# Kernel tuning notes

Measured on AMD Instinct MI355X. Metric: run time of the kernel, lower is better.

The kernel has to match this reference:

```python
import jax, jax.numpy as jnp
import numpy as np

ALPHA = 1.702
LIMIT = 7.0
TOP_K = 2
B, S, H, E, I = 2, 1024, 768, 8, 768


def setup_inputs() -> dict:
    key = jax.random.key(0)
    ks = jax.random.split(key, 7)
    scale = 0.02
    return {
        "hidden_states": jax.random.normal(ks[0], (B, S, H), dtype=jnp.float32),
        "Wr": jax.random.normal(ks[1], (H, E), dtype=jnp.float32) * scale,
        "br": jax.random.normal(ks[2], (E,), dtype=jnp.float32) * scale,
        "Wgu": jax.random.normal(ks[3], (E, H, 2 * I), dtype=jnp.float32) * scale,
        "bgu": jax.random.normal(ks[4], (E, 2 * I), dtype=jnp.float32) * scale,
        "Wd": jax.random.normal(ks[5], (E, I, H), dtype=jnp.float32) * scale,
        "bd": jax.random.normal(ks[6], (E, H), dtype=jnp.float32) * scale,
    }


def reference(hidden_states, Wr, br, Wgu, bgu, Wd, bd):
    # Router: top-K experts per token, softmax over the K selected logits
    logits = jnp.einsum("bsh,he->bse", hidden_states, Wr) + br
    topk_vals, topk_idx = jax.lax.top_k(logits, TOP_K)        # [B,S,K]
    router_scores = jax.nn.softmax(topk_vals, axis=-1)         # [B,S,K]

    # Dense-over-experts grouped GEMM (sparse_matmul reference: unselected
    # experts are computed but never read by the combine gather below).
    gu = jnp.einsum("bsh,ehf->bsef", hidden_states, Wgu) + bgu  # [B,S,E,2I]
    gu = jnp.minimum(gu, LIMIT)
    gate = gu[..., :I]
    up = jnp.maximum(gu[..., I:], -LIMIT)
    glu = gate * jax.nn.sigmoid(gate * ALPHA)
    activated = (up + 1.0) * glu                                # [B,S,E,I]

    down = jnp.einsum("bsei,eih->bseh", activated, Wd) + bd     # [B,S,E,H]

    # all_to_all_combine (num_devices=1): gather this token's K expert outputs
    sel = jnp.take_along_axis(down, topk_idx[..., None], axis=2)  # [B,S,K,H]
    output = jnp.sum(sel * router_scores[..., None], axis=2)      # [B,S,H]
    return output
```

## Files before the change

kernel.cpp:

```cpp
#include <hip/hip_runtime.h>
#include <hip/hip_bf16.h>
#include <cmath>

#define ALPHA 1.702f
#define LIMIT 7.0f

constexpr int B = 2, S = 1024, H = 768, E = 8, I = 768;
constexpr int T = B * S;
constexpr int TWO_I = 2 * I;
constexpr int CAP = T;
constexpr int NT1 = I / 64;
constexpr int NT2 = H / 64;
constexpr int MT = CAP / 128;

constexpr int RTR_BLKS = 64;
constexpr int WGU_TILES = E * (TWO_I / 64) * (H / 64);
constexpr int WD_TILES  = E * (H / 64) * (H / 64);
constexpr int PRE_BLKS = RTR_BLKS + WGU_TILES + WD_TILES;

typedef __attribute__((ext_vector_type(8))) short short8;
typedef __attribute__((ext_vector_type(4))) float floatx4;

__device__ __forceinline__ unsigned short f2bf(float v) {
  __hip_bfloat16 h = __float2bfloat16(v);
  return *reinterpret_cast<unsigned short*>(&h);
}

__device__ __forceinline__ void g2l16(const void* g, void* l) {
  __builtin_amdgcn_global_load_lds(
      (const __attribute__((address_space(1))) void*)g,
      (__attribute__((address_space(3))) void*)l, 16, 0, 0);
}

__global__ __launch_bounds__(256) void fused_pre(
    const float* __restrict__ x, const float* __restrict__ Wr,
    const float* __restrict__ br, const float* __restrict__ Wgu,
    const float* __restrict__ Wd, unsigned short* __restrict__ Wgt,
    unsigned short* __restrict__ Wdt, unsigned short* __restrict__ xb,
    float* __restrict__ out, int* __restrict__ e_cnt,
    int* __restrict__ row_token, float* __restrict__ row_w) {
  int bid = blockIdx.x;
  int tid = threadIdx.x;

  if (bid < RTR_BLKS) {
    __shared__ int cnt_s[E];
    __shared__ int base_s[E];
    __shared__ int tok_e[E][64];
    __shared__ float wv_e[E][64];

    if (tid < E) cnt_s[tid] = 0;
    __syncthreads();

    int wave = tid >> 6;
    int lane = tid & 63;

    for (int tt = 0; tt < 8; tt++) {
      int t = bid * 32 + wave * 8 + tt;
      const float* xr = x + (size_t)t * H;

      float4 z4 = {0.f, 0.f, 0.f, 0.f};
#pragma unroll
      for (int j = 0; j < 3; j++)
        *(float4*)(out + (size_t)t * H + (size_t)(j * 64 + lane) * 4) = z4;

      float acc[E];
#pragma unroll
      for (int e = 0; e < E; e++) acc[e] = 0.0f;

#pragma unroll
      for (int it = 0; it < 3; it++) {
        int h4 = it * 64 + lane;
        float4 xv = *(const float4*)(xr + (size_t)h4 * 4);
        ushort4 xo;
        xo.x = f2bf(xv.x);
        xo.y = f2bf(xv.y);
        xo.z = f2bf(xv.z);
        xo.w = f2bf(xv.w);
        *(ushort4*)(xb + (size_t)t * H + (size_t)h4 * 4) = xo;
        const float* wrow = Wr + (size_t)h4 * 4 * E;
        float xs[4] = {xv.x, xv.y, xv.z, xv.w};
#pragma unroll
        for (int j = 0; j < 4; j++)
#pragma unroll
          for (int e = 0; e < E; e++) acc[e] += xs[j] * wrow[j * E + e];
      }
#pragma unroll
      for (int e = 0; e < E; e++) {
        float v = acc[e];
        for (int off = 32; off > 0; off >>= 1) v += __shfl_down(v, off, 64);
        acc[e] = v;
      }
      if (lane == 0) {
        float logits[E];
#pragma unroll
        for (int e = 0; e < E; e++) logits[e] = acc[e] + br[e];
        int i0 = 0;
        float v0 = logits[0];
#pragma unroll
        for (int e = 1; e < E; e++)
          if (logits[e] > v0) { v0 = logits[e]; i0 = e; }
        int i1 = -1;
        float v1 = -INFINITY;
#pragma unroll
        for (int e = 0; e < E; e++) {
          if (e == i0) continue;
          if (logits[e] > v1) { v1 = logits[e]; i1 = e; }
        }
        float s1 = __expf(v1 - v0);
        float denom = 1.0f + s1;
        int p0 = atomicAdd(&cnt_s[i0], 1);
        tok_e[i0][p0] = t;
        wv_e[i0][p0] = 1.0f / denom;
        int p1 = atomicAdd(&cnt_s[i1], 1);
        tok_e[i1][p1] = t;
        wv_e[i1][p1] = s1 / denom;
      }
    }
    __syncthreads();
    if (tid < E) base_s[tid] = atomicAdd(&e_cnt[tid], cnt_s[tid]);
    __syncthreads();
#pragma unroll
    for (int e = 0; e < E; e++) {
      int c = cnt_s[e], b0 = base_s[e];
      for (int j = tid; j < c; j += 256) {
        row_token[e * CAP + b0 + j] = tok_e[e][j];
        row_w[e * CAP + b0 + j] = wv_e[e][j];
      }
    }
    return;
  }

  int q = bid - RTR_BLKS;
  const float* in;
  unsigned short* outw;
  int N, n0, k0;
  if (q < WGU_TILES) {
    int e = q / 288, rem = q % 288;
    N = TWO_I;
    n0 = (rem % 24) * 64;
    k0 = (rem / 24) * 64;
    in = Wgu + (size_t)e * H * TWO_I;
    outw = Wgt + (size_t)e * TWO_I * H;
  } else {
    int q2 = q - WGU_TILES;
    int e = q2 / 144, rem = q2 % 144;
    N = H;
    n0 = (rem % 12) * 64;
    k0 = (rem / 12) * 64;
    in = Wd + (size_t)e * H * I;
    outw = Wdt + (size_t)e * H * I;
  }
  constexpr int K = 768;

  __shared__ float tile[64][65];
  int jr = tid & 15, r0 = tid >> 4;
#pragma unroll
  for (int p = 0; p < 4; p++) {
    int k = r0 + p * 16;
    float4 v = *(const float4*)(in + (size_t)(k0 + k) * N + n0 + jr * 4);
    tile[k][jr * 4 + 0] = v.x;
    tile[k][jr * 4 + 1] = v.y;
    tile[k][jr * 4 + 2] = v.z;
    tile[k][jr * 4 + 3] = v.w;
  }
  __syncthreads();
#pragma unroll
  for (int p = 0; p < 4; p++) {
    int n = r0 + p * 16;
    ushort4 o;
    o.x = f2bf(tile[jr * 4 + 0][n]);
    o.y = f2bf(tile[jr * 4 + 1][n]);
    o.z = f2bf(tile[jr * 4 + 2][n]);
    o.w = f2bf(tile[jr * 4 + 3][n]);
    *(ushort4*)(outw + (size_t)(n0 + n) * K + k0 + jr * 4) = o;
  }
}

__global__ __launch_bounds__(256) void gemm_gu_mfma(
    const unsigned short* __restrict__ xb, const unsigned short* __restrict__ Wgt,
    const float* __restrict__ bgu, const int* __restrict__ e_cnt,
    const int* __restrict__ row_token, unsigned short* __restrict__ act) {
  int bid = blockIdx.x;
  int g = bid % (E * NT1);
  int mt = bid / (E * NT1);
  int e = g / NT1;
  int n0 = (g % NT1) * 64;
  int cnt = e_cnt[e];
  int m0 = mt * 128;
  if (m0 >= cnt) return;
  int start = e * CAP;
  const unsigned short* Wg = Wgt + (size_t)e * TWO_I * H;
  const float* bias = bgu + (size_t)e * TWO_I;

  __shared__ short As[2][128 * 64];
  __shared__ short Bg[2][64 * 64];
  __shared__ short Bu[2][64 * 64];
  __shared__ int tok[128];

  int tid = threadIdx.x;
  if (tid < 128) {
    int m = m0 + tid;
    tok[tid] = row_token[start + ((m < cnt) ? m : (cnt - 1))];
  }
  __syncthreads();

  int lane = tid & 63;
  int wave = tid >> 6;
  int quad = lane >> 4;
  int lrow = lane & 15;
  int wm = (wave >> 1) * 64;
  int wn = (wave & 1) * 32;

  const unsigned short* gA[4];
  int oA[4];
#pragma unroll
  for (int r = 0; r < 4; r++) {
    int s = (wave * 4 + r) * 64 + lane;
    int row = s >> 3;
    int gg = (s & 7) ^ (row & 7);
    gA[r] = xb + (size_t)tok[row] * H + gg * 8;
    oA[r] = (wave * 4 + r) * 64 * 8;
  }
  const unsigned short *gBg[2], *gBu[2];
  int oB[2];
#pragma unroll
  for (int r = 0; r < 2; r++) {
    int s = (wave * 2 + r) * 64 + lane;
    int row = s >> 3;
    int gg = (s & 7) ^ (row & 7);
    gBg[r] = Wg + (size_t)(n0 + row) * H + gg * 8;
    gBu[r] = gBg[r] + (size_t)I * H;
    oB[r] = (wave * 2 + r) * 64 * 8;
  }

  float bgv[2], buv[2];
#pragma unroll
  for (int tj = 0; tj < 2; tj++) {
    int ncol = n0 + wn + tj * 16 + lrow;
    bgv[tj] = bias[ncol];
    buv[tj] = bias[I + ncol];
  }

  floatx4 accg[4][2], accu[4][2];
#pragma unroll
  for (int i = 0; i < 4; i++)
#pragma unroll
    for (int j = 0; j < 2; j++) {
      accg[i][j] = floatx4{0.f, 0.f, 0.f, 0.f};
      accu[i][j] = floatx4{0.f, 0.f, 0.f, 0.f};
    }

  __syncthreads();

#pragma unroll
  for (int r = 0; r < 4; r++) g2l16(gA[r], &As[0][oA[r]]);
#pragma unroll
  for (int r = 0; r < 2; r++) {
    g2l16(gBg[r], &Bg[0][oB[r]]);
    g2l16(gBu[r], &Bu[0][oB[r]]);
  }

  constexpr int NK = H / 64;
  for (int i = 0; i < NK; i++) {
    int cb = i & 1;
    if (i + 1 < NK) {
      int nb = cb ^ 1;
      int k1 = (i + 1) * 64;
#pragma unroll
      for (int r = 0; r < 4; r++) g2l16(gA[r] + k1, &As[nb][oA[r]]);
#pragma unroll
      for (int r = 0; r < 2; r++) {
        g2l16(gBg[r] + k1, &Bg[nb][oB[r]]);
        g2l16(gBu[r] + k1, &Bu[nb][oB[r]]);
      }
      asm volatile("s_waitcnt vmcnt(8)" ::: "memory");
    } else {
      asm volatile("s_waitcnt vmcnt(0)" ::: "memory");
    }
    __builtin_amdgcn_s_barrier();

#pragma unroll
    for (int ks = 0; ks < 2; ks++) {
      int c = ks * 4 + quad;
      short8 a[4], bg[2], bu[2];
#pragma unroll
      for (int ti = 0; ti < 4; ti++) {
        int r = wm + ti * 16 + lrow;
        a[ti] = *(const short8*)(&As[cb][(r * 8 + (c ^ (r & 7))) * 8]);
      }
#pragma unroll
      for (int tj = 0; tj < 2; tj++) {
        int r = wn + tj * 16 + lrow;
        bg[tj] = *(const short8*)(&Bg[cb][(r * 8 + (c ^ (r & 7))) * 8]);
        bu[tj] = *(const short8*)(&Bu[cb][(r * 8 + (c ^ (r & 7))) * 8]);
      }
#pragma unroll
      for (int ti = 0; ti < 4; ti++)
#pragma unroll
        for (int tj = 0; tj < 2; tj++) {
          accg[ti][tj] = __builtin_amdgcn_mfma_f32_16x16x32_bf16(
              a[ti], bg[tj], accg[ti][tj], 0, 0, 0);
          accu[ti][tj] = __builtin_amdgcn_mfma_f32_16x16x32_bf16(
              a[ti], bu[tj], accu[ti][tj], 0, 0, 0);
        }
    }
    __builtin_amdgcn_s_barrier();
  }

#pragma unroll
  for (int ti = 0; ti < 4; ti++) {
#pragma unroll
    for (int tj = 0; tj < 2; tj++) {
      int ncol = n0 + wn + tj * 16 + lrow;
#pragma unroll
      for (int r = 0; r < 4; r++) {
        int m = m0 + wm + ti * 16 + quad * 4 + r;
        if (m < cnt) {
          float gg = accg[ti][tj][r] + bgv[tj];
          float u = accu[ti][tj][r] + buv[tj];
          gg = fminf(gg, LIMIT);
          u = fmaxf(fminf(u, LIMIT), -LIMIT);
          float glu = gg / (1.0f + __expf(-ALPHA * gg));
          act[(size_t)(start + m) * I + ncol] = f2bf((u + 1.0f) * glu);
        }
      }
    }
  }
}

__global__ __launch_bounds__(256) void gemm_down_mfma(
    const unsigned short* __restrict__ act, const unsigned short* __restrict__ Wdt,
    const float* __restrict__ bd, const int* __restrict__ e_cnt,
    const int* __restrict__ row_token, const float* __restrict__ row_w,
    float* __restrict__ out) {
  int bid = blockIdx.x;
  int g = bid % (E * NT2);
  int mt = bid / (E * NT2);
  int e = g / NT2;
  int n0 = (g % NT2) * 64;
  int cnt = e_cnt[e];
  int m0 = mt * 128;
  if (m0 >= cnt) return;
  int start = e * CAP;
  const unsigned short* Wd = Wdt + (size_t)e * H * I;
  const float* bias = bd + (size_t)e * H;

  __shared__ short As[2][128 * 64];
  __shared__ short Bs[2][64 * 64];
  __shared__ int tok[128];
  __shared__ float wts[128];

  int tid = threadIdx.x;
  if (tid < 128) {
    int m = m0 + tid;
    int mm = (m < cnt) ? m : (cnt - 1);
    tok[tid] = row_token[start + mm];
    wts[tid] = row_w[start + mm];
  }
  __syncthreads();

  int lane = tid & 63;
  int wave = tid >> 6;
  int quad = lane >> 4;
  int lrow = lane & 15;
  int wm = (wave >> 1) * 64;
  int wn = (wave & 1) * 32;

  const unsigned short* gA[4];
  int oA[4];
#pragma unroll
  for (int r = 0; r < 4; r++) {
    int s = (wave * 4 + r) * 64 + lane;
    int row = s >> 3;
    int gg = (s & 7) ^ (row & 7);
    int gm = m0 + row;
    int mm = (gm < cnt) ? gm : (cnt - 1);
    gA[r] = act + (size_t)(start + mm) * I + gg * 8;
    oA[r] = (wave * 4 + r) * 64 * 8;
  }
  const unsigned short* gB[2];
  int oB[2];
#pragma unroll
  for (int r = 0; r < 2; r++) {
    int s = (wave * 2 + r) * 64 + lane;
    int row = s >> 3;
    int gg = (s & 7) ^ (row & 7);
    gB[r] = Wd + (size_t)(n0 + row) * I + gg * 8;
    oB[r] = (wave * 2 + r) * 64 * 8;
  }

  float bdv[2];
#pragma unroll
  for (int tj = 0; tj < 2; tj++) bdv[tj] = bias[n0 + wn + tj * 16 + lrow];

  floatx4 acc[4][2];
#pragma unroll
  for (int i = 0; i < 4; i++)
#pragma unroll
    for (int j = 0; j < 2; j++) acc[i][j] = floatx4{0.f, 0.f, 0.f, 0.f};

  __syncthreads();

#pragma unroll
  for (int r = 0; r < 4; r++) g2l16(gA[r], &As[0][oA[r]]);
#pragma unroll
  for (int r = 0; r < 2; r++) g2l16(gB[r], &Bs[0][oB[r]]);

  constexpr int NK = I / 64;
  for (int i = 0; i < NK; i++) {
    int cb = i & 1;
    if (i + 1 < NK) {
      int nb = cb ^ 1;
      int k1 = (i + 1) * 64;
#pragma unroll
      for (int r = 0; r < 4; r++) g2l16(gA[r] + k1, &As[nb][oA[r]]);
#pragma unroll
      for (int r = 0; r < 2; r++) g2l16(gB[r] + k1, &Bs[nb][oB[r]]);
      asm volatile("s_waitcnt vmcnt(6)" ::: "memory");
    } else {
      asm volatile("s_waitcnt vmcnt(0)" ::: "memory");
    }
    __builtin_amdgcn_s_barrier();

#pragma unroll
    for (int ks = 0; ks < 2; ks++) {
      int c = ks * 4 + quad;
      short8 a[4], b[2];
#pragma unroll
      for (int ti = 0; ti < 4; ti++) {
        int r = wm + ti * 16 + lrow;
        a[ti] = *(const short8*)(&As[cb][(r * 8 + (c ^ (r & 7))) * 8]);
      }
#pragma unroll
      for (int tj = 0; tj < 2; tj++) {
        int r = wn + tj * 16 + lrow;
        b[tj] = *(const short8*)(&Bs[cb][(r * 8 + (c ^ (r & 7))) * 8]);
      }
#pragma unroll
      for (int ti = 0; ti < 4; ti++)
#pragma unroll
        for (int tj = 0; tj < 2; tj++)
          acc[ti][tj] = __builtin_amdgcn_mfma_f32_16x16x32_bf16(
              a[ti], b[tj], acc[ti][tj], 0, 0, 0);
    }
    __builtin_amdgcn_s_barrier();
  }

#pragma unroll
  for (int ti = 0; ti < 4; ti++) {
#pragma unroll
    for (int tj = 0; tj < 2; tj++) {
      int ncol = n0 + wn + tj * 16 + lrow;
#pragma unroll
      for (int r = 0; r < 4; r++) {
        int ml = wm + ti * 16 + quad * 4 + r;
        int m = m0 + ml;
        if (m < cnt) {
          atomicAdd(&out[(size_t)tok[ml] * H + ncol],
                    wts[ml] * (acc[ti][tj][r] + bdv[tj]));
        }
      }
    }
  }
}

extern "C" void kernel_launch(void* const* d_in, const int* in_sizes, int n_in,
                              void* d_out, int out_size, void* d_ws,
                              size_t ws_size, hipStream_t stream) {
  const float* x   = (const float*)d_in[0];
  const float* Wr  = (const float*)d_in[1];
  const float* br  = (const float*)d_in[2];
  const float* Wgu = (const float*)d_in[3];
  const float* bgu = (const float*)d_in[4];
  const float* Wd  = (const float*)d_in[5];
  const float* bd  = (const float*)d_in[6];
  float* out = (float*)d_out;

  char* w = (char*)d_ws;
  int* e_cnt = (int*)w;       w += 16 * sizeof(int);
  int* row_token = (int*)w;   w += (size_t)E * CAP * sizeof(int);
  float* row_w = (float*)w;   w += (size_t)E * CAP * sizeof(float);
  unsigned short* xb  = (unsigned short*)w; w += (size_t)T * H * 2;
  unsigned short* Wgt = (unsigned short*)w; w += (size_t)E * TWO_I * H * 2;
  unsigned short* Wdt = (unsigned short*)w; w += (size_t)E * H * I * 2;
  unsigned short* act = (unsigned short*)w; w += (size_t)E * CAP * I * 2;

  hipMemsetAsync(e_cnt, 0, 16 * sizeof(int), stream);
  fused_pre<<<PRE_BLKS, 256, 0, stream>>>(
      x, Wr, br, Wgu, Wd, Wgt, Wdt, xb, out, e_cnt, row_token, row_w);
  gemm_gu_mfma<<<dim3(MT * E * NT1), 256, 0, stream>>>(
      xb, Wgt, bgu, e_cnt, row_token, act);
  gemm_down_mfma<<<dim3(MT * E * NT2), 256, 0, stream>>>(
      act, Wdt, bd, e_cnt, row_token, row_w, out);
}
```

Baseline: 163.8 us.

## Widen MoE GEMM N-tiles to 128 and use persistent M-tile loops

Both expert GEMMs move from 128x64 to 128x128 output tiles, which doubles the MFMA work done per A-tile load and halves how often the gathered token rows are re-read. Instead of launching one block per (M-tile, expert, N-tile) and exiting early on empty tiles, each block now strides over M-tiles with a fixed stride of 5. This gives a compact grid of 240 blocks for the gate/up GEMM and 240 for the down GEMM. The trade-offs are much larger LDS and register use: the gate/up kernel holds 32 accumulators and is limited to one block per CU. Routing imbalance across experts can also leave some blocks with more M-tiles than others.

```diff
diff --git a/kernel.cpp b/kernel.cpp
--- a/kernel.cpp
+++ b/kernel.cpp
@@ -9,9 +9,12 @@
 constexpr int T = B * S;
 constexpr int TWO_I = 2 * I;
 constexpr int CAP = T;
-constexpr int NT1 = I / 64;
-constexpr int NT2 = H / 64;
 constexpr int MT = CAP / 128;
+constexpr int NT128_1 = I / 128;
+constexpr int NT128_2 = H / 128;
+constexpr int MTB = 5;
+constexpr int G1_BLKS = E * NT128_1 * MTB;
+constexpr int G2_BLKS = E * NT128_2 * MTB;
 
 constexpr int RTR_BLKS = 64;
 constexpr int WGU_TILES = E * (TWO_I / 64) * (H / 64);
@@ -176,288 +179,294 @@
   }
 }
 
-__global__ __launch_bounds__(256) void gemm_gu_mfma(
+__global__ __launch_bounds__(256, 1) void gemm_gu_mfma(
     const unsigned short* __restrict__ xb, const unsigned short* __restrict__ Wgt,
     const float* __restrict__ bgu, const int* __restrict__ e_cnt,
     const int* __restrict__ row_token, unsigned short* __restrict__ act) {
   int bid = blockIdx.x;
-  int g = bid % (E * NT1);
-  int mt = bid / (E * NT1);
-  int e = g / NT1;
-  int n0 = (g % NT1) * 64;
+  int e = bid & 7;
+  int q = bid >> 3;
+  int nt = q % NT128_1;
+  int mtb = q / NT128_1;
+  int n0 = nt * 128;
   int cnt = e_cnt[e];
-  int m0 = mt * 128;
-  if (m0 >= cnt) return;
   int start = e * CAP;
   const unsigned short* Wg = Wgt + (size_t)e * TWO_I * H;
   const float* bias = bgu + (size_t)e * TWO_I;
 
   __shared__ short As[2][128 * 64];
-  __shared__ short Bg[2][64 * 64];
-  __shared__ short Bu[2][64 * 64];
+  __shared__ short Bg[2][128 * 64];
+  __shared__ short Bu[2][128 * 64];
   __shared__ int tok[128];
 
   int tid = threadIdx.x;
-  if (tid < 128) {
-    int m = m0 + tid;
-    tok[tid] = row_token[start + ((m < cnt) ? m : (cnt - 1))];
-  }
-  __syncthreads();
-
   int lane = tid & 63;
   int wave = tid >> 6;
   int quad = lane >> 4;
   int lrow = lane & 15;
   int wm = (wave >> 1) * 64;
-  int wn = (wave & 1) * 32;
-
-  const unsigned short* gA[4];
-  int oA[4];
+  int wn = (wave & 1) * 64;
+
+  const unsigned short *gBg[4], *gBu[4];
+  int oB[4];
 #pragma unroll
   for (int r = 0; r < 4; r++) {
     int s = (wave * 4 + r) * 64 + lane;
     int row = s >> 3;
     int gg = (s & 7) ^ (row & 7);
-    gA[r] = xb + (size_t)tok[row] * H + gg * 8;
-    oA[r] = (wave * 4 + r) * 64 * 8;
-  }
-  const unsigned short *gBg[2], *gBu[2];
-  int oB[2];
-#pragma unroll
-  for (int r = 0; r < 2; r++) {
-    int s = (wave * 2 + r) * 64 + lane;
-    int row = s >> 3;
-    int gg = (s & 7) ^ (row & 7);
     gBg[r] = Wg + (size_t)(n0 + row) * H + gg * 8;
     gBu[r] = gBg[r] + (size_t)I * H;
-    oB[r] = (wave * 2 + r) * 64 * 8;
-  }
-
-  float bgv[2], buv[2];
-#pragma unroll
-  for (int tj = 0; tj < 2; tj++) {
+    oB[r] = (wave * 4 + r) * 64 * 8;
+  }
+  float bgv[4], buv[4];
+#pragma unroll
+  for (int tj = 0; tj < 4; tj++) {
     int ncol = n0 + wn + tj * 16 + lrow;
     bgv[tj] = bias[ncol];
     buv[tj] = bias[I + ncol];
   }
 
-  floatx4 accg[4][2], accu[4][2];
-#pragma unroll
-  for (int i = 0; i < 4; i++)
-#pragma unroll
-    for (int j = 0; j < 2; j++) {
-      accg[i][j] = floatx4{0.f, 0.f, 0.f, 0.f};
-      accu[i][j] = floatx4{0.f, 0.f, 0.f, 0.f};
-    }
-
-  __syncthreads();
-
-#pragma unroll
-  for (int r = 0; r < 4; r++) g2l16(gA[r], &As[0][oA[r]]);
-#pragma unroll
-  for (int r = 0; r < 2; r++) {
-    g2l16(gBg[r], &Bg[0][oB[r]]);
-    g2l16(gBu[r], &Bu[0][oB[r]]);
-  }
-
-  constexpr int NK = H / 64;
-  for (int i = 0; i < NK; i++) {
-    int cb = i & 1;
-    if (i + 1 < NK) {
-      int nb = cb ^ 1;
-      int k1 = (i + 1) * 64;
-#pragma unroll
-      for (int r = 0; r < 4; r++) g2l16(gA[r] + k1, &As[nb][oA[r]]);
-#pragma unroll
-      for (int r = 0; r < 2; r++) {
-        g2l16(gBg[r] + k1, &Bg[nb][oB[r]]);
-        g2l16(gBu[r] + k1, &Bu[nb][oB[r]]);
-      }
-      asm volatile("s_waitcnt vmcnt(8)" ::: "memory");
-    } else {
-      asm volatile("s_waitcnt vmcnt(0)" ::: "memory");
-    }
-    __builtin_amdgcn_s_barrier();
-
-#pragma unroll
-    for (int ks = 0; ks < 2; ks++) {
-      int c = ks * 4 + quad;
-      short8 a[4], bg[2], bu[2];
-#pragma unroll
-      for (int ti = 0; ti < 4; ti++) {
-        int r = wm + ti * 16 + lrow;
-        a[ti] = *(const short8*)(&As[cb][(r * 8 + (c ^ (r & 7))) * 8]);
-      }
-#pragma unroll
-      for (int tj = 0; tj < 2; tj++) {
-        int r = wn + tj * 16 + lrow;
-        bg[tj] = *(const short8*)(&Bg[cb][(r * 8 + (c ^ (r & 7))) * 8]);
-        bu[tj] = *(const short8*)(&Bu[cb][(r * 8 + (c ^ (r & 7))) * 8]);
-      }
-#pragma unroll
-      for (int ti = 0; ti < 4; ti++)
-#pragma unroll
-        for (int tj = 0; tj < 2; tj++) {
-          accg[ti][tj] = __builtin_amdgcn_mfma_f32_16x16x32_bf16(
-              a[ti], bg[tj], accg[ti][tj], 0, 0, 0);
-          accu[ti][tj] = __builtin_amdgcn_mfma_f32_16x16x32_bf16(
-              a[ti], bu[tj], accu[ti][tj], 0, 0, 0);
-        }
-    }
-    __builtin_amdgcn_s_barrier();
-  }
-
-#pragma unroll
-  for (int ti = 0; ti < 4; ti++) {
-#pragma unroll
-    for (int tj = 0; tj < 2; tj++) {
-      int ncol = n0 + wn + tj * 16 + lrow;
-#pragma unroll
-      for (int r = 0; r < 4; r++) {
-        int m = m0 + wm + ti * 16 + quad * 4 + r;
-        if (m < cnt) {
-          float gg = accg[ti][tj][r] + bgv[tj];
-          float u = accu[ti][tj][r] + buv[tj];
-          gg = fminf(gg, LIMIT);
-          u = fmaxf(fminf(u, LIMIT), -LIMIT);
-          float glu = gg / (1.0f + __expf(-ALPHA * gg));
-          act[(size_t)(start + m) * I + ncol] = f2bf((u + 1.0f) * glu);
+  for (int mt = mtb; mt < MT; mt += MTB) {
+    int m0 = mt * 128;
+    if (m0 >= cnt) continue;
+
+    __syncthreads();
+    if (tid < 128) {
+      int m = m0 + tid;
+      tok[tid] = row_token[start + ((m < cnt) ? m : (cnt - 1))];
+    }
+    __syncthreads();
+
+    const unsigned short* gA[4];
+    int oA[4];
+#pragma unroll
+    for (int r = 0; r < 4; r++) {
+      int s = (wave * 4 + r) * 64 + lane;
+      int row = s >> 3;
+      int gg = (s & 7) ^ (row & 7);
+      gA[r] = xb + (size_t)tok[row] * H + gg * 8;
+      oA[r] = (wave * 4 + r) * 64 * 8;
+    }
+
+    floatx4 accg[4][4], accu[4][4];
+#pragma unroll
+    for (int i = 0; i < 4; i++)
+#pragma unroll
+      for (int j = 0; j < 4; j++) {
+        accg[i][j] = floatx4{0.f, 0.f, 0.f, 0.f};
+        accu[i][j] = floatx4{0.f, 0.f, 0.f, 0.f};
+      }
+
+#pragma unroll
+    for (int r = 0; r < 4; r++) g2l16(gA[r], &As[0][oA[r]]);
+#pragma unroll
+    for (int r = 0; r < 4; r++) {
+      g2l16(gBg[r], &Bg[0][oB[r]]);
+      g2l16(gBu[r], &Bu[0][oB[r]]);
+    }
+
+    constexpr int NK = H / 64;
+    for (int i = 0; i < NK; i++) {
+      int cb = i & 1;
+      if (i + 1 < NK) {
+        int nb = cb ^ 1;
+        int k1 = (i + 1) * 64;
+#pragma unroll
+        for (int r = 0; r < 4; r++) g2l16(gA[r] + k1, &As[nb][oA[r]]);
+#pragma unroll
+        for (int r = 0; r < 4; r++) {
+          g2l16(gBg[r] + k1, &Bg[nb][oB[r]]);
+          g2l16(gBu[r] + k1, &Bu[nb][oB[r]]);
+        }
+        asm volatile("s_waitcnt vmcnt(12)" ::: "memory");
+      } else {
+        asm volatile("s_waitcnt vmcnt(0)" ::: "memory");
+      }
+      __builtin_amdgcn_s_barrier();
+
+#pragma unroll
+      for (int ks = 0; ks < 2; ks++) {
+        int c = ks * 4 + quad;
+        short8 a[4], bg[4], bu[4];
+#pragma unroll
+        for (int ti = 0; ti < 4; ti++) {
+          int r = wm + ti * 16 + lrow;
+          a[ti] = *(const short8*)(&As[cb][(r * 8 + (c ^ (r & 7))) * 8]);
+        }
+#pragma unroll
+        for (int tj = 0; tj < 4; tj++) {
+          int r = wn + tj * 16 + lrow;
+          bg[tj] = *(const short8*)(&Bg[cb][(r * 8 + (c ^ (r & 7))) * 8]);
+          bu[tj] = *(const short8*)(&Bu[cb][(r * 8 + (c ^ (r & 7))) * 8]);
+        }
+#pragma unroll
+        for (int ti = 0; ti < 4; ti++)
+#pragma unroll
+          for (int tj = 0; tj < 4; tj++) {
+            accg[ti][tj] = __builtin_amdgcn_mfma_f32_16x16x32_bf16(
+                a[ti], bg[tj], accg[ti][tj], 0, 0, 0);
+            accu[ti][tj] = __builtin_amdgcn_mfma_f32_16x16x32_bf16(
+                a[ti], bu[tj], accu[ti][tj], 0, 0, 0);
+          }
+      }
+      __builtin_amdgcn_s_barrier();
+    }
+
+#pragma unroll
+    for (int ti = 0; ti < 4; ti++) {
+#pragma unroll
+      for (int tj = 0; tj < 4; tj++) {
+        int ncol = n0 + wn + tj * 16 + lrow;
+#pragma unroll
+        for (int r = 0; r < 4; r++) {
+          int m = m0 + wm + ti * 16 + quad * 4 + r;
+          if (m < cnt) {
+            float gg = accg[ti][tj][r] + bgv[tj];
+            float u = accu[ti][tj][r] + buv[tj];
+            gg = fminf(gg, LIMIT);
+            u = fmaxf(fminf(u, LIMIT), -LIMIT);
+            float glu = gg / (1.0f + __expf(-ALPHA * gg));
+            act[(size_t)(start + m) * I + ncol] = f2bf((u + 1.0f) * glu);
+          }
         }
       }
     }
   }
 }
 
-__global__ __launch_bounds__(256) void gemm_down_mfma(
+__global__ __launch_bounds__(256, 2) void gemm_down_mfma(
     const unsigned short* __restrict__ act, const unsigned short* __restrict__ Wdt,
     const float* __restrict__ bd, const int* __restrict__ e_cnt,
     const int* __restrict__ row_token, const float* __restrict__ row_w,
     float* __restrict__ out) {
   int bid = blockIdx.x;
-  int g = bid % (E * NT2);
-  int mt = bid / (E * NT2);
-  int e = g / NT2;
-  int n0 = (g % NT2) * 64;
+  int e = bid & 7;
+  int q = bid >> 3;
+  int nt = q % NT128_2;
+  int mtb = q / NT128_2;
+  int n0 = nt * 128;
   int cnt = e_cnt[e];
-  int m0 = mt * 128;
-  if (m0 >= cnt) return;
   int start = e * CAP;
   const unsigned short* Wd = Wdt + (size_t)e * H * I;
   const float* bias = bd + (size_t)e * H;
 
   __shared__ short As[2][128 * 64];
-  __shared__ short Bs[2][64 * 64];
+  __shared__ short Bs[2][128 * 64];
   __shared__ int tok[128];
   __shared__ float wts[128];
 
   int tid = threadIdx.x;
-  if (tid < 128) {
-    int m = m0 + tid;
-    int mm = (m < cnt) ? m : (cnt - 1);
-    tok[tid] = row_token[start + mm];
-    wts[tid] = row_w[start + mm];
-  }
-  __syncthreads();
-
   int lane = tid & 63;
   int wave = tid >> 6;
   int quad = lane >> 4;
   int lrow = lane & 15;
   int wm = (wave >> 1) * 64;
-  int wn = (wave & 1) * 32;
-
-  const unsigned short* gA[4];
-  int oA[4];
+  int wn = (wave & 1) * 64;
+
+  const unsigned short* gB[4];
+  int oB[4];
 #pragma unroll
   for (int r = 0; r < 4; r++) {
     int s = (wave * 4 + r) * 64 + lane;
     int row = s >> 3;
     int gg = (s & 7) ^ (row & 7);
-    int gm = m0 + row;
-    int mm = (gm < cnt) ? gm : (cnt - 1);
-    gA[r] = act + (size_t)(start + mm) * I + gg * 8;
-    oA[r] = (wave * 4 + r) * 64 * 8;
-  }
-  const unsigned short* gB[2];
-  int oB[2];
-#pragma unroll
-  for (int r = 0; r < 2; r++) {
-    int s = (wave * 2 + r) * 64 + lane;
-    int row = s >> 3;
-    int gg = (s & 7) ^ (row & 7);
     gB[r] = Wd + (size_t)(n0 + row) * I + gg * 8;
-    oB[r] = (wave * 2 + r) * 64 * 8;
-  }
-
-  float bdv[2];
-#pragma unroll
-  for (int tj = 0; tj < 2; tj++) bdv[tj] = bias[n0 + wn + tj * 16 + lrow];
-
-  floatx4 acc[4][2];
-#pragma unroll
-  for (int i = 0; i < 4; i++)
-#pragma unroll
-    for (int j = 0; j < 2; j++) acc[i][j] = floatx4{0.f, 0.f, 0.f, 0.f};
-
-  __syncthreads();
-
-#pragma unroll
-  for (int r = 0; r < 4; r++) g2l16(gA[r], &As[0][oA[r]]);
-#pragma unroll
-  for (int r = 0; r < 2; r++) g2l16(gB[r], &Bs[0][oB[r]]);
-
-  constexpr int NK = I / 64;
-  for (int i = 0; i < NK; i++) {
-    int cb = i & 1;
-    if (i + 1 < NK) {
-      int nb = cb ^ 1;
-      int k1 = (i + 1) * 64;
-#pragma unroll
-      for (int r = 0; r < 4; r++) g2l16(gA[r] + k1, &As[nb][oA[r]]);
-#pragma unroll
-      for (int r = 0; r < 2; r++) g2l16(gB[r] + k1, &Bs[nb][oB[r]]);
-      asm volatile("s_waitcnt vmcnt(6)" ::: "memory");
-    } else {
-      asm volatile("s_waitcnt vmcnt(0)" ::: "memory");
-    }
-    __builtin_amdgcn_s_barrier();
-
-#pragma unroll
-    for (int ks = 0; ks < 2; ks++) {
-      int c = ks * 4 + quad;
-      short8 a[4], b[2];
-#pragma unroll
-      for (int ti = 0; ti < 4; ti++) {
-        int r = wm + ti * 16 + lrow;
-        a[ti] = *(const short8*)(&As[cb][(r * 8 + (c ^ (r & 7))) * 8]);
-      }
-#pragma unroll
-      for (int tj = 0; tj < 2; tj++) {
-        int r = wn + tj * 16 + lrow;
-        b[tj] = *(const short8*)(&Bs[cb][(r * 8 + (c ^ (r & 7))) * 8]);
-      }
-#pragma unroll
-      for (int ti = 0; ti < 4; ti++)
-#pragma unroll
-        for (int tj = 0; tj < 2; tj++)
-          acc[ti][tj] = __builtin_amdgcn_mfma_f32_16x16x32_bf16(
-              a[ti], b[tj], acc[ti][tj], 0, 0, 0);
-    }
-    __builtin_amdgcn_s_barrier();
-  }
-
-#pragma unroll
-  for (int ti = 0; ti < 4; ti++) {
-#pragma unroll
-    for (int tj = 0; tj < 2; tj++) {
-      int ncol = n0 + wn + tj * 16 + lrow;
-#pragma unroll
-      for (int r = 0; r < 4; r++) {
-        int ml = wm + ti * 16 + quad * 4 + r;
-        int m = m0 + ml;
-        if (m < cnt) {
-          atomicAdd(&out[(size_t)tok[ml] * H + ncol],
-                    wts[ml] * (acc[ti][tj][r] + bdv[tj]));
+    oB[r] = (wave * 4 + r) * 64 * 8;
+  }
+  float bdv[4];
+#pragma unroll
+  for (int tj = 0; tj < 4; tj++) bdv[tj] = bias[n0 + wn + tj * 16 + lrow];
+
+  for (int mt = mtb; mt < MT; mt += MTB) {
+    int m0 = mt * 128;
+    if (m0 >= cnt) continue;
+
+    __syncthreads();
+    if (tid < 128) {
+      int m = m0 + tid;
+      int mm = (m < cnt) ? m : (cnt - 1);
+      tok[tid] = row_token[start + mm];
+      wts[tid] = row_w[start + mm];
+    }
+    __syncthreads();
+
+    const unsigned short* gA[4];
+    int oA[4];
+#pragma unroll
+    for (int r = 0; r < 4; r++) {
+      int s = (wave * 4 + r) * 64 + lane;
+      int row = s >> 3;
+      int gg = (s & 7) ^ (row & 7);
+      int gm = m0 + row;
+      int mm = (gm < cnt) ? gm : (cnt - 1);
+      gA[r] = act + (size_t)(start + mm) * I + gg * 8;
+      oA[r] = (wave * 4 + r) * 64 * 8;
+    }
+
+    floatx4 acc[4][4];
+#pragma unroll
+    for (int i = 0; i < 4; i++)
+#pragma unroll
+      for (int j = 0; j < 4; j++) acc[i][j] = floatx4{0.f, 0.f, 0.f, 0.f};
+
+#pragma unroll
+    for (int r = 0; r < 4; r++) g2l16(gA[r], &As[0][oA[r]]);
+#pragma unroll
+    for (int r = 0; r < 4; r++) g2l16(gB[r], &Bs[0][oB[r]]);
+
+    constexpr int NK = I / 64;
+    for (int i = 0; i < NK; i++) {
+      int cb = i & 1;
+      if (i + 1 < NK) {
+        int nb = cb ^ 1;
+        int k1 = (i + 1) * 64;
+#pragma unroll
+        for (int r = 0; r < 4; r++) g2l16(gA[r] + k1, &As[nb][oA[r]]);
+#pragma unroll
+        for (int r = 0; r < 4; r++) g2l16(gB[r] + k1, &Bs[nb][oB[r]]);
+        asm volatile("s_waitcnt vmcnt(8)" ::: "memory");
+      } else {
+        asm volatile("s_waitcnt vmcnt(0)" ::: "memory");
+      }
+      __builtin_amdgcn_s_barrier();
+
+#pragma unroll
+      for (int ks = 0; ks < 2; ks++) {
+        int c = ks * 4 + quad;
+        short8 a[4], b[4];
+#pragma unroll
+        for (int ti = 0; ti < 4; ti++) {
+          int r = wm + ti * 16 + lrow;
+          a[ti] = *(const short8*)(&As[cb][(r * 8 + (c ^ (r & 7))) * 8]);
+        }
+#pragma unroll
+        for (int tj = 0; tj < 4; tj++) {
+          int r = wn + tj * 16 + lrow;
+          b[tj] = *(const short8*)(&Bs[cb][(r * 8 + (c ^ (r & 7))) * 8]);
+        }
+#pragma unroll
+        for (int ti = 0; ti < 4; ti++)
+#pragma unroll
+          for (int tj = 0; tj < 4; tj++)
+            acc[ti][tj] = __builtin_amdgcn_mfma_f32_16x16x32_bf16(
+                a[ti], b[tj], acc[ti][tj], 0, 0, 0);
+      }
+      __builtin_amdgcn_s_barrier();
+    }
+
+#pragma unroll
+    for (int ti = 0; ti < 4; ti++) {
+#pragma unroll
+      for (int tj = 0; tj < 4; tj++) {
+        int ncol = n0 + wn + tj * 16 + lrow;
+#pragma unroll
+        for (int r = 0; r < 4; r++) {
+          int ml = wm + ti * 16 + quad * 4 + r;
+          int m = m0 + ml;
+          if (m < cnt) {
+            atomicAdd(&out[(size_t)tok[ml] * H + ncol],
+                      wts[ml] * (acc[ti][tj][r] + bdv[tj]));
+          }
         }
       }
     }
@@ -488,8 +497,8 @@
   hipMemsetAsync(e_cnt, 0, 16 * sizeof(int), stream);
   fused_pre<<<PRE_BLKS, 256, 0, stream>>>(
       x, Wr, br, Wgu, Wd, Wgt, Wdt, xb, out, e_cnt, row_token, row_w);
-  gemm_gu_mfma<<<dim3(MT * E * NT1), 256, 0, stream>>>(
+  gemm_gu_mfma<<<dim3(G1_BLKS), 256, 0, stream>>>(
       xb, Wgt, bgu, e_cnt, row_token, act);
-  gemm_down_mfma<<<dim3(MT * E * NT2), 256, 0, stream>>>(
+  gemm_down_mfma<<<dim3(G2_BLKS), 256, 0, stream>>>(
       act, Wdt, bd, e_cnt, row_token, row_w, out);
 }
```

Result: slower. 169.6 us (+3.6%).

## Move Wd transpose into gate-up GEMM launch to overlap with compute

Applied to the files above, without the earlier changes.

The down-projection weight transpose/bf16 conversion is moved out of the pre-processing kernel and appended as extra blocks to the gate-up GEMM kernel. Those blocks do not depend on the router output, so they can fill idle CUs while the GEMM runs, which shortens the serial pre-processing stage. Shared memory is now a union of the GEMM buffers and the transpose tile. The cost is extra blocks competing with GEMM tiles for bandwidth and CUs.

```diff
diff --git a/kernel.cpp b/kernel.cpp
--- a/kernel.cpp
+++ b/kernel.cpp
@@ -16,7 +16,10 @@
 constexpr int RTR_BLKS = 64;
 constexpr int WGU_TILES = E * (TWO_I / 64) * (H / 64);
 constexpr int WD_TILES  = E * (H / 64) * (H / 64);
-constexpr int PRE_BLKS = RTR_BLKS + WGU_TILES + WD_TILES;
+constexpr int PRE_BLKS = RTR_BLKS + WGU_TILES;
+constexpr int G1_BLKS = MT * E * NT1;
+constexpr int K1_BLKS = G1_BLKS + WD_TILES;
+constexpr int G2_BLKS = MT * E * NT2;
 
 typedef __attribute__((ext_vector_type(8))) short short8;
 typedef __attribute__((ext_vector_type(4))) float floatx4;
@@ -32,11 +35,37 @@
       (__attribute__((address_space(3))) void*)l, 16, 0, 0);
 }
 
-__global__ __launch_bounds__(256) void fused_pre(
+__device__ __forceinline__ void transpose_tile(
+    const float* __restrict__ in, unsigned short* __restrict__ outw,
+    int N, int n0, int k0, float (*tile)[65], int tid) {
+  constexpr int K = 768;
+  int jr = tid & 15, r0 = tid >> 4;
+#pragma unroll
+  for (int p = 0; p < 4; p++) {
+    int k = r0 + p * 16;
+    float4 v = *(const float4*)(in + (size_t)(k0 + k) * N + n0 + jr * 4);
+    tile[k][jr * 4 + 0] = v.x;
+    tile[k][jr * 4 + 1] = v.y;
+    tile[k][jr * 4 + 2] = v.z;
+    tile[k][jr * 4 + 3] = v.w;
+  }
+  __syncthreads();
+#pragma unroll
+  for (int p = 0; p < 4; p++) {
+    int n = r0 + p * 16;
+    ushort4 o;
+    o.x = f2bf(tile[jr * 4 + 0][n]);
+    o.y = f2bf(tile[jr * 4 + 1][n]);
+    o.z = f2bf(tile[jr * 4 + 2][n]);
+    o.w = f2bf(tile[jr * 4 + 3][n]);
+    *(ushort4*)(outw + (size_t)(n0 + n) * K + k0 + jr * 4) = o;
+  }
+}
+
+__global__ __launch_bounds__(256) void pre_router_wgu(
     const float* __restrict__ x, const float* __restrict__ Wr,
     const float* __restrict__ br, const float* __restrict__ Wgu,
-    const float* __restrict__ Wd, unsigned short* __restrict__ Wgt,
-    unsigned short* __restrict__ Wdt, unsigned short* __restrict__ xb,
+    unsigned short* __restrict__ Wgt, unsigned short* __restrict__ xb,
     float* __restrict__ out, int* __restrict__ e_cnt,
     int* __restrict__ row_token, float* __restrict__ row_w) {
   int bid = blockIdx.x;
@@ -130,57 +159,46 @@
     return;
   }
 
+  __shared__ float tile[64][65];
   int q = bid - RTR_BLKS;
-  const float* in;
-  unsigned short* outw;
-  int N, n0, k0;
-  if (q < WGU_TILES) {
-    int e = q / 288, rem = q % 288;
-    N = TWO_I;
-    n0 = (rem % 24) * 64;
-    k0 = (rem / 24) * 64;
-    in = Wgu + (size_t)e * H * TWO_I;
-    outw = Wgt + (size_t)e * TWO_I * H;
-  } else {
-    int q2 = q - WGU_TILES;
-    int e = q2 / 144, rem = q2 % 144;
-    N = H;
-    n0 = (rem % 12) * 64;
-    k0 = (rem / 12) * 64;
-    in = Wd + (size_t)e * H * I;
-    outw = Wdt + (size_t)e * H * I;
-  }
-  constexpr int K = 768;
-
-  __shared__ float tile[64][65];
-  int jr = tid & 15, r0 = tid >> 4;
-#pragma unroll
-  for (int p = 0; p < 4; p++) {
-    int k = r0 + p * 16;
-    float4 v = *(const float4*)(in + (size_t)(k0 + k) * N + n0 + jr * 4);
-    tile[k][jr * 4 + 0] = v.x;
-    tile[k][jr * 4 + 1] = v.y;
-    tile[k][jr * 4 + 2] = v.z;
-    tile[k][jr * 4 + 3] = v.w;
-  }
-  __syncthreads();
-#pragma unroll
-  for (int p = 0; p < 4; p++) {
-    int n = r0 + p * 16;
-    ushort4 o;
-    o.x = f2bf(tile[jr * 4 + 0][n]);
-    o.y = f2bf(tile[jr * 4 + 1][n]);
-    o.z = f2bf(tile[jr * 4 + 2][n]);
-    o.w = f2bf(tile[jr * 4 + 3][n]);
-    *(ushort4*)(outw + (size_t)(n0 + n) * K + k0 + jr * 4) = o;
-  }
-}
-
-__global__ __launch_bounds__(256) void gemm_gu_mfma(
+  int e = q / 288, rem = q % 288;
+  int n0 = (rem % 24) * 64;
+  int k0 = (rem / 24) * 64;
+  transpose_tile(Wgu + (size_t)e * H * TWO_I, Wgt + (size_t)e * TWO_I * H,
+                 TWO_I, n0, k0, tile, tid);
+}
+
+struct G1Smem {
+  short As[2][128 * 64];
+  short Bg[2][64 * 64];
+  short Bu[2][64 * 64];
+  int tok[128];
+};
+struct TSmem {
+  float tile[64][65];
+};
+
+__global__ __launch_bounds__(256) void gemm_gu_wdT(
     const unsigned short* __restrict__ xb, const unsigned short* __restrict__ Wgt,
     const float* __restrict__ bgu, const int* __restrict__ e_cnt,
-    const int* __restrict__ row_token, unsigned short* __restrict__ act) {
+    const int* __restrict__ row_token, unsigned short* __restrict__ act,
+    const float* __restrict__ Wd, unsigned short* __restrict__ Wdt) {
+  __shared__ __align__(16) char smem_raw[sizeof(G1Smem)];
   int bid = blockIdx.x;
+  int tid = threadIdx.x;
+
+  if (bid >= G1_BLKS) {
+    TSmem* ts = (TSmem*)smem_raw;
+    int q = bid - G1_BLKS;
+    int e = q / 144, rem = q % 144;
+    int n0 = (rem % 12) * 64;
+    int k0 = (rem / 12) * 64;
+    transpose_tile(Wd + (size_t)e * H * I, Wdt + (size_t)e * H * I,
+                   H, n0, k0, ts->tile, tid);
+    return;
+  }
+
+  G1Smem* sm = (G1Smem*)smem_raw;
   int g = bid % (E * NT1);
   int mt = bid / (E * NT1);
   int e = g / NT1;
@@ -192,15 +210,9 @@
   const unsigned short* Wg = Wgt + (size_t)e * TWO_I * H;
   const float* bias = bgu + (size_t)e * TWO_I;
 
-  __shared__ short As[2][128 * 64];
-  __shared__ short Bg[2][64 * 64];
-  __shared__ short Bu[2][64 * 64];
-  __shared__ int tok[128];
-
-  int tid = threadIdx.x;
   if (tid < 128) {
     int m = m0 + tid;
-    tok[tid] = row_token[start + ((m < cnt) ? m : (cnt - 1))];
+    sm->tok[tid] = row_token[start + ((m < cnt) ? m : (cnt - 1))];
   }
   __syncthreads();
 
@@ -218,7 +230,7 @@
     int s = (wave * 4 + r) * 64 + lane;
     int row = s >> 3;
     int gg = (s & 7) ^ (row & 7);
-    gA[r] = xb + (size_t)tok[row] * H + gg * 8;
+    gA[r] = xb + (size_t)sm->tok[row] * H + gg * 8;
     oA[r] = (wave * 4 + r) * 64 * 8;
   }
   const unsigned short *gBg[2], *gBu[2];
@@ -253,11 +265,11 @@
   __syncthreads();
 
 #pragma unroll
-  for (int r = 0; r < 4; r++) g2l16(gA[r], &As[0][oA[r]]);
+  for (int r = 0; r < 4; r++) g2l16(gA[r], &sm->As[0][oA[r]]);
 #pragma unroll
   for (int r = 0; r < 2; r++) {
-    g2l16(gBg[r], &Bg[0][oB[r]]);
-    g2l16(gBu[r], &Bu[0][oB[r]]);
+    g2l16(gBg[r], &sm->Bg[0][oB[r]]);
+    g2l16(gBu[r], &sm->Bu[0][oB[r]]);
   }
 
   constexpr int NK = H / 64;
@@ -267,11 +279,11 @@
       int nb = cb ^ 1;
       int k1 = (i + 1) * 64;
 #pragma unroll
-      for (int r = 0; r < 4; r++) g2l16(gA[r] + k1, &As[nb][oA[r]]);
+      for (int r = 0; r < 4; r++) g2l16(gA[r] + k1, &sm->As[nb][oA[r]]);
 #pragma unroll
       for (int r = 0; r < 2; r++) {
-        g2l16(gBg[r] + k1, &Bg[nb][oB[r]]);
-        g2l16(gBu[r] + k1, &Bu[nb][oB[r]]);
+        g2l16(gBg[r] + k1, &sm->Bg[nb][oB[r]]);
+        g2l16(gBu[r] + k1, &sm->Bu[nb][oB[r]]);
       }
       asm volatile("s_waitcnt vmcnt(8)" ::: "memory");
     } else {
@@ -286,13 +298,13 @@
 #pragma unroll
       for (int ti = 0; ti < 4; ti++) {
         int r = wm + ti * 16 + lrow;
-        a[ti] = *(const short8*)(&As[cb][(r * 8 + (c ^ (r & 7))) * 8]);
+        a[ti] = *(const short8*)(&sm->As[cb][(r * 8 + (c ^ (r & 7))) * 8]);
       }
 #pragma unroll
       for (int tj = 0; tj < 2; tj++) {
         int r = wn + tj * 16 + lrow;
-        bg[tj] = *(const short8*)(&Bg[cb][(r * 8 + (c ^ (r & 7))) * 8]);
-        bu[tj] = *(const short8*)(&Bu[cb][(r * 8 + (c ^ (r & 7))) * 8]);
+        bg[tj] = *(const short8*)(&sm->Bg[cb][(r * 8 + (c ^ (r & 7))) * 8]);
+        bu[tj] = *(const short8*)(&sm->Bu[cb][(r * 8 + (c ^ (r & 7))) * 8]);
       }
 #pragma unroll
       for (int ti = 0; ti < 4; ti++)
@@ -486,10 +498,10 @@
   unsigned short* act = (unsigned short*)w; w += (size_t)E * CAP * I * 2;
 
   hipMemsetAsync(e_cnt, 0, 16 * sizeof(int), stream);
-  fused_pre<<<PRE_BLKS, 256, 0, stream>>>(
-      x, Wr, br, Wgu, Wd, Wgt, Wdt, xb, out, e_cnt, row_token, row_w);
-  gemm_gu_mfma<<<dim3(MT * E * NT1), 256, 0, stream>>>(
-      xb, Wgt, bgu, e_cnt, row_token, act);
-  gemm_down_mfma<<<dim3(MT * E * NT2), 256, 0, stream>>>(
+  pre_router_wgu<<<PRE_BLKS, 256, 0, stream>>>(
+      x, Wr, br, Wgu, Wgt, xb, out, e_cnt, row_token, row_w);
+  gemm_gu_wdT<<<K1_BLKS, 256, 0, stream>>>(
+      xb, Wgt, bgu, e_cnt, row_token, act, Wd, Wdt);
+  gemm_down_mfma<<<G2_BLKS, 256, 0, stream>>>(
       act, Wdt, bd, e_cnt, row_token, row_w, out);
 }
```

New measurement: 162.8 us. No clear change (-0.6%).

## Split down-proj K across blocks, write partials to buffer, reduce without atomics

Applied to the files above, without the earlier changes.

The down-projection GEMM now splits its K dimension in half, doubling the block count. Each block writes its weighted partial result to a per-(token, slot, k-half) scratch buffer instead of doing float atomicAdd into the output. A new reduce kernel sums the four partials per token, which also removes the need to zero the output in the prologue. The router now uses smaller blocks and encodes the slot in the token index. This trades atomics and low occupancy for an extra kernel launch and a 25 MB scratch round trip.

```diff
diff --git a/kernel.cpp b/kernel.cpp
--- a/kernel.cpp
+++ b/kernel.cpp
@@ -12,11 +12,15 @@
 constexpr int NT1 = I / 64;
 constexpr int NT2 = H / 64;
 constexpr int MT = CAP / 128;
-
-constexpr int RTR_BLKS = 64;
+constexpr int KH = I / 2;
+
+constexpr int RTR_BLKS = 128;
 constexpr int WGU_TILES = E * (TWO_I / 64) * (H / 64);
 constexpr int WD_TILES  = E * (H / 64) * (H / 64);
 constexpr int PRE_BLKS = RTR_BLKS + WGU_TILES + WD_TILES;
+constexpr int G1_BLKS = MT * E * NT1;
+constexpr int G2_BLKS = 2 * MT * E * NT2;
+constexpr int RED_BLKS = (T * H / 4) / 256;
 
 typedef __attribute__((ext_vector_type(8))) short short8;
 typedef __attribute__((ext_vector_type(4))) float floatx4;
@@ -32,21 +36,48 @@
       (__attribute__((address_space(3))) void*)l, 16, 0, 0);
 }
 
-__global__ __launch_bounds__(256) void fused_pre(
+__device__ __forceinline__ void transpose_tile(
+    const float* __restrict__ in, unsigned short* __restrict__ outw,
+    int N, int n0, int k0, float (*tile)[65], int tid) {
+  constexpr int K = 768;
+  int jr = tid & 15, r0 = tid >> 4;
+#pragma unroll
+  for (int p = 0; p < 4; p++) {
+    int k = r0 + p * 16;
+    float4 v = *(const float4*)(in + (size_t)(k0 + k) * N + n0 + jr * 4);
+    tile[k][jr * 4 + 0] = v.x;
+    tile[k][jr * 4 + 1] = v.y;
+    tile[k][jr * 4 + 2] = v.z;
+    tile[k][jr * 4 + 3] = v.w;
+  }
+  __syncthreads();
+#pragma unroll
+  for (int p = 0; p < 4; p++) {
+    int n = r0 + p * 16;
+    ushort4 o;
+    o.x = f2bf(tile[jr * 4 + 0][n]);
+    o.y = f2bf(tile[jr * 4 + 1][n]);
+    o.z = f2bf(tile[jr * 4 + 2][n]);
+    o.w = f2bf(tile[jr * 4 + 3][n]);
+    *(ushort4*)(outw + (size_t)(n0 + n) * K + k0 + jr * 4) = o;
+  }
+}
+
+__global__ __launch_bounds__(256) void pre_all(
     const float* __restrict__ x, const float* __restrict__ Wr,
     const float* __restrict__ br, const float* __restrict__ Wgu,
     const float* __restrict__ Wd, unsigned short* __restrict__ Wgt,
     unsigned short* __restrict__ Wdt, unsigned short* __restrict__ xb,
-    float* __restrict__ out, int* __restrict__ e_cnt,
-    int* __restrict__ row_token, float* __restrict__ row_w) {
+    int* __restrict__ e_cnt, int* __restrict__ row_token,
+    float* __restrict__ row_w) {
   int bid = blockIdx.x;
   int tid = threadIdx.x;
 
   if (bid < RTR_BLKS) {
     __shared__ int cnt_s[E];
     __shared__ int base_s[E];
-    __shared__ int tok_e[E][64];
-    __shared__ float wv_e[E][64];
+    __shared__ int tok_e[E][32];
+    __shared__ float wv_e[E][32];
 
     if (tid < E) cnt_s[tid] = 0;
     __syncthreads();
@@ -54,14 +85,9 @@
     int wave = tid >> 6;
     int lane = tid & 63;
 
-    for (int tt = 0; tt < 8; tt++) {
-      int t = bid * 32 + wave * 8 + tt;
+    for (int tt = 0; tt < 4; tt++) {
+      int t = bid * 16 + wave * 4 + tt;
       const float* xr = x + (size_t)t * H;
-
-      float4 z4 = {0.f, 0.f, 0.f, 0.f};
-#pragma unroll
-      for (int j = 0; j < 3; j++)
-        *(float4*)(out + (size_t)t * H + (size_t)(j * 64 + lane) * 4) = z4;
 
       float acc[E];
 #pragma unroll
@@ -109,10 +135,10 @@
         float s1 = __expf(v1 - v0);
         float denom = 1.0f + s1;
         int p0 = atomicAdd(&cnt_s[i0], 1);
-        tok_e[i0][p0] = t;
+        tok_e[i0][p0] = t * 2 + 0;
         wv_e[i0][p0] = 1.0f / denom;
         int p1 = atomicAdd(&cnt_s[i1], 1);
-        tok_e[i1][p1] = t;
+        tok_e[i1][p1] = t * 2 + 1;
         wv_e[i1][p1] = s1 / denom;
       }
     }
@@ -130,49 +156,21 @@
     return;
   }
 
+  __shared__ float tile[64][65];
   int q = bid - RTR_BLKS;
-  const float* in;
-  unsigned short* outw;
-  int N, n0, k0;
   if (q < WGU_TILES) {
     int e = q / 288, rem = q % 288;
-    N = TWO_I;
-    n0 = (rem % 24) * 64;
-    k0 = (rem / 24) * 64;
-    in = Wgu + (size_t)e * H * TWO_I;
-    outw = Wgt + (size_t)e * TWO_I * H;
+    int n0 = (rem % 24) * 64;
+    int k0 = (rem / 24) * 64;
+    transpose_tile(Wgu + (size_t)e * H * TWO_I, Wgt + (size_t)e * TWO_I * H,
+                   TWO_I, n0, k0, tile, tid);
   } else {
     int q2 = q - WGU_TILES;
     int e = q2 / 144, rem = q2 % 144;
-    N = H;
-    n0 = (rem % 12) * 64;
-    k0 = (rem / 12) * 64;
-    in = Wd + (size_t)e * H * I;
-    outw = Wdt + (size_t)e * H * I;
-  }
-  constexpr int K = 768;
-
-  __shared__ float tile[64][65];
-  int jr = tid & 15, r0 = tid >> 4;
-#pragma unroll
-  for (int p = 0; p < 4; p++) {
-    int k = r0 + p * 16;
-    float4 v = *(const float4*)(in + (size_t)(k0 + k) * N + n0 + jr * 4);
-    tile[k][jr * 4 + 0] = v.x;
-    tile[k][jr * 4 + 1] = v.y;
-    tile[k][jr * 4 + 2] = v.z;
-    tile[k][jr * 4 + 3] = v.w;
-  }
-  __syncthreads();
-#pragma unroll
-  for (int p = 0; p < 4; p++) {
-    int n = r0 + p * 16;
-    ushort4 o;
-    o.x = f2bf(tile[jr * 4 + 0][n]);
-    o.y = f2bf(tile[jr * 4 + 1][n]);
-    o.z = f2bf(tile[jr * 4 + 2][n]);
-    o.w = f2bf(tile[jr * 4 + 3][n]);
-    *(ushort4*)(outw + (size_t)(n0 + n) * K + k0 + jr * 4) = o;
+    int n0 = (rem % 12) * 64;
+    int k0 = (rem / 12) * 64;
+    transpose_tile(Wd + (size_t)e * H * I, Wdt + (size_t)e * H * I,
+                   H, n0, k0, tile, tid);
   }
 }
 
@@ -180,7 +178,13 @@
     const unsigned short* __restrict__ xb, const unsigned short* __restrict__ Wgt,
     const float* __restrict__ bgu, const int* __restrict__ e_cnt,
     const int* __restrict__ row_token, unsigned short* __restrict__ act) {
+  __shared__ short As[2][128 * 64];
+  __shared__ short Bg[2][64 * 64];
+  __shared__ short Bu[2][64 * 64];
+  __shared__ int tok[128];
   int bid = blockIdx.x;
+  int tid = threadIdx.x;
+
   int g = bid % (E * NT1);
   int mt = bid / (E * NT1);
   int e = g / NT1;
@@ -192,12 +196,6 @@
   const unsigned short* Wg = Wgt + (size_t)e * TWO_I * H;
   const float* bias = bgu + (size_t)e * TWO_I;
 
-  __shared__ short As[2][128 * 64];
-  __shared__ short Bg[2][64 * 64];
-  __shared__ short Bu[2][64 * 64];
-  __shared__ int tok[128];
-
-  int tid = threadIdx.x;
   if (tid < 128) {
     int m = m0 + tid;
     tok[tid] = row_token[start + ((m < cnt) ? m : (cnt - 1))];
@@ -218,7 +216,7 @@
     int s = (wave * 4 + r) * 64 + lane;
     int row = s >> 3;
     int gg = (s & 7) ^ (row & 7);
-    gA[r] = xb + (size_t)tok[row] * H + gg * 8;
+    gA[r] = xb + (size_t)(tok[row] >> 1) * H + gg * 8;
     oA[r] = (wave * 4 + r) * 64 * 8;
   }
   const unsigned short *gBg[2], *gBu[2];
@@ -332,25 +330,28 @@
     const unsigned short* __restrict__ act, const unsigned short* __restrict__ Wdt,
     const float* __restrict__ bd, const int* __restrict__ e_cnt,
     const int* __restrict__ row_token, const float* __restrict__ row_w,
-    float* __restrict__ out) {
+    float* __restrict__ down) {
+  __shared__ short As[2][128 * 64];
+  __shared__ short Bs[2][64 * 64];
+  __shared__ int tok[128];
+  __shared__ float wts[128];
   int bid = blockIdx.x;
+  int tid = threadIdx.x;
+
   int g = bid % (E * NT2);
-  int mt = bid / (E * NT2);
+  int q = bid / (E * NT2);
+  int kp = q & 1;
+  int mt = q >> 1;
   int e = g / NT2;
   int n0 = (g % NT2) * 64;
   int cnt = e_cnt[e];
   int m0 = mt * 128;
   if (m0 >= cnt) return;
   int start = e * CAP;
+  int k_off = kp * KH;
   const unsigned short* Wd = Wdt + (size_t)e * H * I;
   const float* bias = bd + (size_t)e * H;
 
-  __shared__ short As[2][128 * 64];
-  __shared__ short Bs[2][64 * 64];
-  __shared__ int tok[128];
-  __shared__ float wts[128];
-
-  int tid = threadIdx.x;
   if (tid < 128) {
     int m = m0 + tid;
     int mm = (m < cnt) ? m : (cnt - 1);
@@ -375,7 +376,7 @@
     int gg = (s & 7) ^ (row & 7);
     int gm = m0 + row;
     int mm = (gm < cnt) ? gm : (cnt - 1);
-    gA[r] = act + (size_t)(start + mm) * I + gg * 8;
+    gA[r] = act + (size_t)(start + mm) * I + k_off + gg * 8;
     oA[r] = (wave * 4 + r) * 64 * 8;
   }
   const unsigned short* gB[2];
@@ -385,13 +386,14 @@
     int s = (wave * 2 + r) * 64 + lane;
     int row = s >> 3;
     int gg = (s & 7) ^ (row & 7);
-    gB[r] = Wd + (size_t)(n0 + row) * I + gg * 8;
+    gB[r] = Wd + (size_t)(n0 + row) * I + k_off + gg * 8;
     oB[r] = (wave * 2 + r) * 64 * 8;
   }
 
   float bdv[2];
 #pragma unroll
-  for (int tj = 0; tj < 2; tj++) bdv[tj] = bias[n0 + wn + tj * 16 + lrow];
+  for (int tj = 0; tj < 2; tj++)
+    bdv[tj] = kp ? 0.0f : bias[n0 + wn + tj * 16 + lrow];
 
   floatx4 acc[4][2];
 #pragma unroll
@@ -406,7 +408,7 @@
 #pragma unroll
   for (int r = 0; r < 2; r++) g2l16(gB[r], &Bs[0][oB[r]]);
 
-  constexpr int NK = I / 64;
+  constexpr int NK = KH / 64;
   for (int i = 0; i < NK; i++) {
     int cb = i & 1;
     if (i + 1 < NK) {
@@ -456,12 +458,27 @@
         int ml = wm + ti * 16 + quad * 4 + r;
         int m = m0 + ml;
         if (m < cnt) {
-          atomicAdd(&out[(size_t)tok[ml] * H + ncol],
-                    wts[ml] * (acc[ti][tj][r] + bdv[tj]));
+          down[((size_t)tok[ml] * 2 + kp) * H + ncol] =
+              wts[ml] * (acc[ti][tj][r] + bdv[tj]);
         }
       }
     }
   }
+}
+
+__global__ __launch_bounds__(256) void reduce_out(
+    const float* __restrict__ down, float* __restrict__ out) {
+  int i4 = blockIdx.x * 256 + threadIdx.x;
+  int t = i4 / (H / 4);
+  int c = i4 % (H / 4);
+  const float* base = down + (size_t)(4 * t) * H;
+  float4 r0 = ((const float4*)(base + 0 * H))[c];
+  float4 r1 = ((const float4*)(base + 1 * H))[c];
+  float4 r2 = ((const float4*)(base + 2 * H))[c];
+  float4 r3 = ((const float4*)(base + 3 * H))[c];
+  float4 r = {r0.x + r1.x + r2.x + r3.x, r0.y + r1.y + r2.y + r3.y,
+              r0.z + r1.z + r2.z + r3.z, r0.w + r1.w + r2.w + r3.w};
+  ((float4*)(out + (size_t)t * H))[c] = r;
 }
 
 extern "C" void kernel_launch(void* const* d_in, const int* in_sizes, int n_in,
@@ -484,12 +501,14 @@
   unsigned short* Wgt = (unsigned short*)w; w += (size_t)E * TWO_I * H * 2;
   unsigned short* Wdt = (unsigned short*)w; w += (size_t)E * H * I * 2;
   unsigned short* act = (unsigned short*)w; w += (size_t)E * CAP * I * 2;
+  float* down = (float*)w;    w += (size_t)T * 4 * H * sizeof(float);
 
   hipMemsetAsync(e_cnt, 0, 16 * sizeof(int), stream);
-  fused_pre<<<PRE_BLKS, 256, 0, stream>>>(
-      x, Wr, br, Wgu, Wd, Wgt, Wdt, xb, out, e_cnt, row_token, row_w);
-  gemm_gu_mfma<<<dim3(MT * E * NT1), 256, 0, stream>>>(
+  pre_all<<<PRE_BLKS, 256, 0, stream>>>(
+      x, Wr, br, Wgu, Wd, Wgt, Wdt, xb, e_cnt, row_token, row_w);
+  gemm_gu_mfma<<<G1_BLKS, 256, 0, stream>>>(
       xb, Wgt, bgu, e_cnt, row_token, act);
-  gemm_down_mfma<<<dim3(MT * E * NT2), 256, 0, stream>>>(
-      act, Wdt, bd, e_cnt, row_token, row_w, out);
-}
+  gemm_down_mfma<<<G2_BLKS, 256, 0, stream>>>(
+      act, Wdt, bd, e_cnt, row_token, row_w, down);
+  reduce_out<<<RED_BLKS, 256, 0, stream>>>(down, out);
+}
```

After: 161.8 us. No clear change (-1.2%).
